# Optimization experiments

Measured on AMD Instinct MI355X. Metric: run time of the kernel, lower is better.

Reference implementation:

```python
import jax, jax.numpy as jnp
import numpy as np

B, S, D_IN, D_OUT = 4, 2048, 1024, 1024
USE_MASK = True


def setup_inputs() -> dict:
    key = jax.random.key(0)
    ks = jax.random.split(key, 6)
    return {
        "inputs_for_keys": jax.random.normal(ks[0], (B, S, D_IN), jnp.float32),
        "inputs_for_values": jax.random.normal(ks[1], (B, S, D_IN), jnp.float32),
        "inputs_for_queries": jax.random.normal(ks[2], (B, S, D_IN), jnp.float32),
        "WK": jax.random.normal(ks[3], (D_IN, D_OUT), jnp.float32) * 0.1,
        "WV": jax.random.normal(ks[4], (D_IN, D_OUT), jnp.float32) * 0.1,
        "WQ": jax.random.normal(ks[5], (D_IN, D_OUT), jnp.float32) * 0.1,
    }


def reference(inputs_for_keys, inputs_for_values, inputs_for_queries, WK, WV, WQ):
    # projections: [B,S,Din] @ [Din,Dout] -> [B,S,Dout]
    K = jnp.einsum("bsd,de->bse", inputs_for_keys, WK)
    V = jnp.einsum("bsd,de->bse", inputs_for_values, WV)
    Q = jnp.einsum("bsd,de->bse", inputs_for_queries, WQ)

    dk = jnp.asarray(K.shape[2], jnp.float32)
    # scores: [B, Sq, Sk]
    score = jnp.einsum("bqd,bkd->bqk", Q, K) / jnp.sqrt(dk)
    if USE_MASK:
        # causal: -inf strictly above diagonal (j > i), matching the
        # transposed tril(-1) * -inf construction in the original.
        q_idx = jnp.arange(S)[:, None]
        k_idx = jnp.arange(S)[None, :]
        mask = jnp.where(k_idx > q_idx, -jnp.inf, 0.0).astype(score.dtype)
        score = score + mask[None, :, :]
    soft_score = jax.nn.softmax(score, axis=-1)
    return jnp.einsum("bqk,bkd->bqd", soft_score, V)
```

## Files before the change

### kernel.cpp

```cpp
#include <hip/hip_runtime.h>
#include <hip/hip_bf16.h>

typedef unsigned short u16;
typedef _Float16 f16;
typedef __attribute__((ext_vector_type(8))) short s16x8;
typedef __attribute__((ext_vector_type(8))) _Float16 f16x8;
typedef __attribute__((ext_vector_type(4))) float f32x4;
typedef __attribute__((ext_vector_type(4))) unsigned short u16x4;

template <typename T>
__device__ __forceinline__ auto mfma_try(T a, T b, f32x4 c, int)
    -> decltype(__builtin_amdgcn_mfma_f32_16x16x32_f16(a, b, c, 0, 0, 0)) {
  return __builtin_amdgcn_mfma_f32_16x16x32_f16(a, b, c, 0, 0, 0);
}
template <typename T>
__device__ __forceinline__ f32x4 mfma_try(T a, T b, f32x4 c, long) {
  return __builtin_amdgcn_mfma_f32_16x16x32_f16(
      __builtin_bit_cast(f16x8, a), __builtin_bit_cast(f16x8, b), c, 0, 0, 0);
}
__device__ __forceinline__ f32x4 MFMA16(s16x8 a, s16x8 b, f32x4 c) {
  return mfma_try(a, b, c, 0);
}

__device__ __forceinline__ void gload16(const void* g, void* s) {
  __builtin_amdgcn_global_load_lds(
      (const __attribute__((address_space(1))) void*)g,
      (__attribute__((address_space(3))) void*)s, 16, 0, 0);
}

__device__ __forceinline__ u16 f2h(float x) {
  f16 h = (f16)x;
  u16 u;
  __builtin_memcpy(&u, &h, 2);
  return u;
}
__device__ __forceinline__ float h2f(u16 u) {
  f16 h;
  __builtin_memcpy(&h, &u, 2);
  return (float)h;
}

#define LDS_SWZ(r, cb) ((cb) ^ (((r)&7) << 4))

struct Geom {
  int srow[4], scol[4];
  int w, l, wr, wc;
};

__device__ __forceinline__ Geom make_geom() {
  Geom g;
  int tid = threadIdx.x;
  g.w = tid >> 6; g.l = tid & 63;
  g.wr = g.w >> 1; g.wc = g.w & 1;
#pragma unroll
  for (int i = 0; i < 4; ++i) {
    int off = i * 4096 + g.w * 1024 + g.l * 16;
    int r = off >> 7, cb = off & 127;
    g.srow[i] = r;
    g.scol[i] = LDS_SWZ(r, cb) >> 1;
  }
  return g;
}

__device__ __forceinline__ void stage(const u16* pan, int ld, int k0,
                                      char* lds, const Geom& g) {
#pragma unroll
  for (int i = 0; i < 4; ++i)
    gload16(pan + (long)g.srow[i] * ld + k0 + g.scol[i],
            lds + i * 4096 + g.w * 1024);
}

__device__ __forceinline__ void compute_step(const char* lA, const char* lB,
                                             const Geom& g, f32x4 acc[4][4]) {
#pragma unroll
  for (int ks = 0; ks < 2; ++ks) {
    s16x8 af[4], bg[4];
#pragma unroll
    for (int m = 0; m < 4; ++m) {
      int r = g.wr * 64 + m * 16 + (g.l & 15);
      int cb = ks * 64 + ((g.l >> 4) << 4);
      af[m] = *(const s16x8*)(lA + r * 128 + LDS_SWZ(r, cb));
    }
#pragma unroll
    for (int n = 0; n < 4; ++n) {
      int r = g.wc * 64 + n * 16 + (g.l & 15);
      int cb = ks * 64 + ((g.l >> 4) << 4);
      bg[n] = *(const s16x8*)(lB + r * 128 + LDS_SWZ(r, cb));
    }
#pragma unroll
    for (int m = 0; m < 4; ++m)
#pragma unroll
      for (int n = 0; n < 4; ++n)
        acc[m][n] = MFMA16(af[m], bg[n], acc[m][n]);
  }
}

__device__ __forceinline__ void gemm_core(const u16* Apan, int lda,
                                          const u16* Bpan, int ldb, int nsteps,
                                          char* lA, char* lB, const Geom& g,
                                          f32x4 acc[4][4]) {
  stage(Apan, lda, 0, lA, g);
  stage(Bpan, ldb, 0, lB, g);
  __syncthreads();
  for (int t = 0; t < nsteps; ++t) {
    int cur = (t & 1) << 14;
    if (t + 1 < nsteps) {
      int nxt = ((t + 1) & 1) << 14;
      stage(Apan, lda, (t + 1) * 64, lA + nxt, g);
      stage(Bpan, ldb, (t + 1) * 64, lB + nxt, g);
    }
    compute_step(lA + cur, lB + cur, g, acc);
    if (t + 1 < nsteps) __syncthreads();
  }
}

__global__ __launch_bounds__(256, 2) void proj_kernel(
    const u16* __restrict__ xk, const u16* __restrict__ xq, const u16* __restrict__ xv,
    const u16* __restrict__ wk, const u16* __restrict__ wq, const u16* __restrict__ wv,
    u16* __restrict__ K, u16* __restrict__ Q, u16* __restrict__ Vt) {
  __shared__ char lds[65536];
  const int y = blockIdx.y;
  const u16* X = y == 0 ? xk : (y == 1 ? xq : xv);
  const u16* W = y == 0 ? wk : (y == 1 ? wq : wv);
  const int bx = blockIdx.x;
  const int swz = (bx & 7) * 64 + (bx >> 3);
  const int tm = swz >> 3, tn = swz & 7;
  Geom g = make_geom();
  f32x4 acc[4][4] = {};
  gemm_core(X + (long)tm * 128 * 1024, 1024, W + (long)tn * 128 * 1024, 1024,
            16, lds, lds + 32768, g, acc);
  const int rg0 = tm * 128 + g.wr * 64, cg0 = tn * 128 + g.wc * 64;
  if (y < 2) {
    u16* C = y == 0 ? K : Q;
#pragma unroll
    for (int m = 0; m < 4; ++m)
#pragma unroll
      for (int n = 0; n < 4; ++n)
#pragma unroll
        for (int j = 0; j < 4; ++j) {
          int rg = rg0 + m * 16 + ((g.l >> 4) << 2) + j;
          int cg = cg0 + n * 16 + (g.l & 15);
          C[(long)rg * 1024 + cg] = f2h(acc[m][n][j]);
        }
  } else {
#pragma unroll
    for (int m = 0; m < 4; ++m) {
      int rg = rg0 + m * 16 + ((g.l >> 4) << 2);
      int b = rg >> 11, rl = rg & 2047;
#pragma unroll
      for (int n = 0; n < 4; ++n) {
        int cg = cg0 + n * 16 + (g.l & 15);
        u16x4 pk;
#pragma unroll
        for (int j = 0; j < 4; ++j) pk[j] = f2h(acc[m][n][j]);
        *(u16x4*)(Vt + (long)b * (1024 * 2048) + (long)cg * 2048 + rl) = pk;
      }
    }
  }
}

__global__ __launch_bounds__(256, 2) void qkt_kernel(
    const u16* __restrict__ Q, const u16* __restrict__ K, u16* __restrict__ S) {
  __shared__ char lds[65536];
  const int bx = blockIdx.x;
  const int swz = (bx & 7) * 68 + (bx >> 3);
  const int b = swz / 136;
  int t = swz - b * 136;
  int tm = 0;
  while (t > tm) { t -= tm + 1; ++tm; }
  const int tn = t;
  Geom g = make_geom();
  f32x4 acc[4][4] = {};
  const u16* Qb = Q + (long)b * 2048 * 1024;
  const u16* Kb = K + (long)b * 2048 * 1024;
  gemm_core(Qb + (long)tm * 128 * 1024, 1024, Kb + (long)tn * 128 * 1024, 1024,
            16, lds, lds + 32768, g, acc);
  u16* Sb = S + (long)b * 2048 * 2048;
  const int rg0 = tm * 128 + g.wr * 64, cg0 = tn * 128 + g.wc * 64;
#pragma unroll
  for (int m = 0; m < 4; ++m)
#pragma unroll
    for (int n = 0; n < 4; ++n)
#pragma unroll
      for (int j = 0; j < 4; ++j) {
        int rg = rg0 + m * 16 + ((g.l >> 4) << 2) + j;
        int cg = cg0 + n * 16 + (g.l & 15);
        Sb[(long)rg * 2048 + cg] = f2h(acc[m][n][j]);
      }
}

__global__ __launch_bounds__(256, 2) void pv_kernel(
    const u16* __restrict__ P, const u16* __restrict__ Vt, float* __restrict__ O) {
  __shared__ char lds[65536];
  const int bx = blockIdx.x;
  const int swz = (bx & 7) * 64 + (bx >> 3);
  const int b = swz >> 7, loc = swz & 127;
  const int tm = loc >> 3, tn = loc & 7;
  Geom g = make_geom();
  f32x4 acc[4][4] = {};
  gemm_core(P + ((long)b * 2048 + tm * 128) * 2048, 2048,
            Vt + (long)b * 1024 * 2048 + (long)tn * 128 * 2048, 2048,
            (tm + 1) * 2, lds, lds + 32768, g, acc);
  const int rg0 = tm * 128 + g.wr * 64, cg0 = tn * 128 + g.wc * 64;
#pragma unroll
  for (int m = 0; m < 4; ++m)
#pragma unroll
    for (int n = 0; n < 4; ++n)
#pragma unroll
      for (int j = 0; j < 4; ++j) {
        int rg = rg0 + m * 16 + ((g.l >> 4) << 2) + j;
        int cg = cg0 + n * 16 + (g.l & 15);
        O[((long)b * 2048 + rg) * 1024 + cg] = acc[m][n][j];
      }
}

__global__ __launch_bounds__(256) void softmax_causal(
    const u16* __restrict__ S, u16* __restrict__ P) {
  const int row = blockIdx.x;
  const int i_q = row & 2047;
  const u16* sr = S + (long)row * 2048;
  u16* pr = P + (long)row * 2048;
  const int tid = threadIdx.x;
  const int l = tid & 63, w = tid >> 6;
  const int base = tid * 8;

  s16x8 raw = *(const s16x8*)(sr + base);
  float v[8];
  float m = -INFINITY;
#pragma unroll
  for (int j = 0; j < 8; ++j) {
    float x = h2f((u16)raw[j]);
    x = (base + j <= i_q) ? x : -INFINITY;
    v[j] = x;
    m = fmaxf(m, x);
  }
  __shared__ float red[8];
  for (int o = 32; o; o >>= 1) m = fmaxf(m, __shfl_xor(m, o, 64));
  if (l == 0) red[w] = m;
  __syncthreads();
  m = fmaxf(fmaxf(red[0], red[1]), fmaxf(red[2], red[3]));

  float s = 0.f;
#pragma unroll
  for (int j = 0; j < 8; ++j) {
    v[j] = expf(v[j] - m);
    s += v[j];
  }
  for (int o = 32; o; o >>= 1) s += __shfl_xor(s, o, 64);
  if (l == 0) red[4 + w] = s;
  __syncthreads();
  s = (red[4] + red[5]) + (red[6] + red[7]);
  float inv = 1.0f / s;

  s16x8 o;
#pragma unroll
  for (int j = 0; j < 8; ++j) o[j] = (short)f2h(v[j] * inv);
  *(s16x8*)(pr + base) = o;
}

__global__ __launch_bounds__(256) void xcast_kernel(
    const float* __restrict__ x0, const float* __restrict__ x1,
    const float* __restrict__ x2, u16* __restrict__ o0, u16* __restrict__ o1,
    u16* __restrict__ o2) {
  const int y = blockIdx.y;
  const float* in = y == 0 ? x0 : (y == 1 ? x1 : x2);
  u16* out = y == 0 ? o0 : (y == 1 ? o1 : o2);
  long i = ((long)blockIdx.x * 256 + threadIdx.x) * 8;
  f32x4 a = *(const f32x4*)(in + i);
  f32x4 b = *(const f32x4*)(in + i + 4);
  s16x8 o;
#pragma unroll
  for (int j = 0; j < 4; ++j) {
    o[j] = (short)f2h(a[j]);
    o[4 + j] = (short)f2h(b[j]);
  }
  *(s16x8*)(out + i) = o;
}

__global__ __launch_bounds__(256) void wcast_kernel(
    const float* __restrict__ wk, const float* __restrict__ wv,
    const float* __restrict__ wq, u16* __restrict__ ok, u16* __restrict__ ov,
    u16* __restrict__ oq) {
  __shared__ float tile[32][33];
  const int z = blockIdx.z;
  const float* w = z == 0 ? wk : (z == 1 ? wv : wq);
  u16* o = z == 0 ? ok : (z == 1 ? ov : oq);
  const float scale = (z == 2) ? 0.03125f : 1.0f;
  const int bx = blockIdx.x, by = blockIdx.y;
  const int lx = threadIdx.x & 31, ly = threadIdx.x >> 5;
#pragma unroll
  for (int j = 0; j < 32; j += 8)
    tile[ly + j][lx] = w[(long)(by * 32 + ly + j) * 1024 + bx * 32 + lx];
  __syncthreads();
#pragma unroll
  for (int j = 0; j < 32; j += 8)
    o[(long)(bx * 32 + ly + j) * 1024 + by * 32 + lx] = f2h(tile[lx][ly + j] * scale);
}

extern "C" void kernel_launch(void* const* d_in, const int* in_sizes, int n_in,
                              void* d_out, int out_size, void* d_ws, size_t ws_size,
                              hipStream_t stream) {
  const float* Xk = (const float*)d_in[0];
  const float* Xv = (const float*)d_in[1];
  const float* Xq = (const float*)d_in[2];
  const float* WK = (const float*)d_in[3];
  const float* WV = (const float*)d_in[4];
  const float* WQ = (const float*)d_in[5];

  const int Bn = 4, S = 2048, D = 1024;
  const long NX = (long)Bn * S * D;

  const size_t r0 = (size_t)Bn * S * S * 4;
  const size_t r1 = r0 + 3ull * D * D * 2;
  const size_t r2 = r1 + 2ull * NX * 2;
  const size_t NEED = r2 + (size_t)NX * 2;
  if (ws_size < NEED) {
    hipMemsetAsync(d_out, 0, (size_t)out_size * 4, stream);
    return;
  }
  char* ws = (char*)d_ws;
  u16* xkb = (u16*)ws;
  u16* xvb = xkb + NX;
  u16* xqb = xvb + NX;
  u16* scoresH = (u16*)ws;
  u16* wkt = (u16*)(ws + r0);
  u16* wvt = wkt + D * D;
  u16* wqt = wvt + D * D;
  u16* Kb = (u16*)(ws + r1);
  u16* Qb = Kb + NX;
  u16* Pb = (u16*)(ws + r1);
  u16* Vt = (u16*)(ws + r2);

  xcast_kernel<<<dim3(4096, 3), 256, 0, stream>>>(Xk, Xv, Xq, xkb, xvb, xqb);
  wcast_kernel<<<dim3(32, 32, 3), 256, 0, stream>>>(WK, WV, WQ, wkt, wvt, wqt);
  proj_kernel<<<dim3(512, 3), 256, 0, stream>>>(xkb, xqb, xvb, wkt, wqt, wvt,
                                                Kb, Qb, Vt);
  qkt_kernel<<<dim3(544), 256, 0, stream>>>(Qb, Kb, scoresH);
  softmax_causal<<<dim3(8192), 256, 0, stream>>>(scoresH, Pb);
  pv_kernel<<<dim3(512), 256, 0, stream>>>(Pb, Vt, (float*)d_out);
}
```

Before: 163.4 us.

## Fuse input fp32->fp16 cast into projection GEMM, balance causal PV, trim softmax

The projection kernel now loads fp32 activations directly into registers, converts them to fp16 and writes them into swizzled LDS, which removes the separate xcast kernel and its round trip through global memory. The PV kernel pairs row tile p with row tile 15-p in each block, so every block does the same causal work, and it launches half as many blocks. Softmax skips loading fully masked 8-element chunks and only writes P up to the 128-column tile boundary that PV reads. The costs are more register pressure and synchronous register-staged loads in the projection, and a longer serial loop in each PV block.

```diff
diff --git a/kernel.cpp b/kernel.cpp
--- a/kernel.cpp
+++ b/kernel.cpp
@@ -43,7 +43,10 @@
 #define LDS_SWZ(r, cb) ((cb) ^ (((r)&7) << 4))
 
 struct Geom {
-  int srow[4], scol[4];
+  int srow[4];
+  int scol[4];
+  int scnat[4];
+  int wofs[4];
   int w, l, wr, wc;
 };
 
@@ -58,6 +61,8 @@
     int r = off >> 7, cb = off & 127;
     g.srow[i] = r;
     g.scol[i] = LDS_SWZ(r, cb) >> 1;
+    g.scnat[i] = cb >> 1;
+    g.wofs[i] = r * 128 + LDS_SWZ(r, cb);
   }
   return g;
 }
@@ -68,6 +73,29 @@
   for (int i = 0; i < 4; ++i)
     gload16(pan + (long)g.srow[i] * ld + k0 + g.scol[i],
             lds + i * 4096 + g.w * 1024);
+}
+
+__device__ __forceinline__ void a_issue(const float* Xpan, int k0,
+                                        const Geom& g, f32x4 (&ar)[8]) {
+#pragma unroll
+  for (int i = 0; i < 4; ++i) {
+    const float* src = Xpan + (long)g.srow[i] * 1024 + k0 + g.scnat[i];
+    ar[2 * i] = *(const f32x4*)(src);
+    ar[2 * i + 1] = *(const f32x4*)(src + 4);
+  }
+}
+__device__ __forceinline__ void a_write(char* lA, const Geom& g,
+                                        const f32x4 (&ar)[8]) {
+#pragma unroll
+  for (int i = 0; i < 4; ++i) {
+    s16x8 h;
+#pragma unroll
+    for (int j = 0; j < 4; ++j) {
+      h[j] = (short)f2h(ar[2 * i][j]);
+      h[4 + j] = (short)f2h(ar[2 * i + 1][j]);
+    }
+    *(s16x8*)(lA + g.wofs[i]) = h;
+  }
 }
 
 __device__ __forceinline__ void compute_step(const char* lA, const char* lB,
@@ -114,21 +142,46 @@
   }
 }
 
+__device__ __forceinline__ void gemm_core_xf32(const float* Xpan,
+                                               const u16* Bpan, int ldb,
+                                               int nsteps, char* lA, char* lB,
+                                               const Geom& g, f32x4 acc[4][4]) {
+  f32x4 ar[8];
+  a_issue(Xpan, 0, g, ar);
+  stage(Bpan, ldb, 0, lB, g);
+  a_write(lA, g, ar);
+  __syncthreads();
+  for (int t = 0; t < nsteps; ++t) {
+    int cur = (t & 1) << 14;
+    int nxt = ((t + 1) & 1) << 14;
+    if (t + 1 < nsteps) {
+      a_issue(Xpan, (t + 1) * 64, g, ar);
+      stage(Bpan, ldb, (t + 1) * 64, lB + nxt, g);
+    }
+    compute_step(lA + cur, lB + cur, g, acc);
+    if (t + 1 < nsteps) {
+      a_write(lA + nxt, g, ar);
+      __syncthreads();
+    }
+  }
+}
+
 __global__ __launch_bounds__(256, 2) void proj_kernel(
-    const u16* __restrict__ xk, const u16* __restrict__ xq, const u16* __restrict__ xv,
-    const u16* __restrict__ wk, const u16* __restrict__ wq, const u16* __restrict__ wv,
+    const float* __restrict__ xk, const float* __restrict__ xq,
+    const float* __restrict__ xv, const u16* __restrict__ wk,
+    const u16* __restrict__ wq, const u16* __restrict__ wv,
     u16* __restrict__ K, u16* __restrict__ Q, u16* __restrict__ Vt) {
   __shared__ char lds[65536];
   const int y = blockIdx.y;
-  const u16* X = y == 0 ? xk : (y == 1 ? xq : xv);
+  const float* X = y == 0 ? xk : (y == 1 ? xq : xv);
   const u16* W = y == 0 ? wk : (y == 1 ? wq : wv);
   const int bx = blockIdx.x;
   const int swz = (bx & 7) * 64 + (bx >> 3);
   const int tm = swz >> 3, tn = swz & 7;
   Geom g = make_geom();
   f32x4 acc[4][4] = {};
-  gemm_core(X + (long)tm * 128 * 1024, 1024, W + (long)tn * 128 * 1024, 1024,
-            16, lds, lds + 32768, g, acc);
+  gemm_core_xf32(X + (long)tm * 128 * 1024, W + (long)tn * 128 * 1024, 1024,
+                 16, lds, lds + 32768, g, acc);
   const int rg0 = tm * 128 + g.wr * 64, cg0 = tn * 128 + g.wc * 64;
   if (y < 2) {
     u16* C = y == 0 ? K : Q;
@@ -193,46 +246,56 @@
     const u16* __restrict__ P, const u16* __restrict__ Vt, float* __restrict__ O) {
   __shared__ char lds[65536];
   const int bx = blockIdx.x;
-  const int swz = (bx & 7) * 64 + (bx >> 3);
-  const int b = swz >> 7, loc = swz & 127;
-  const int tm = loc >> 3, tn = loc & 7;
+  const int swz = (bx & 7) * 32 + (bx >> 3);
+  const int b = swz >> 6, loc = swz & 63;
+  const int p = loc >> 3, tn = loc & 7;
   Geom g = make_geom();
-  f32x4 acc[4][4] = {};
-  gemm_core(P + ((long)b * 2048 + tm * 128) * 2048, 2048,
-            Vt + (long)b * 1024 * 2048 + (long)tn * 128 * 2048, 2048,
-            (tm + 1) * 2, lds, lds + 32768, g, acc);
-  const int rg0 = tm * 128 + g.wr * 64, cg0 = tn * 128 + g.wc * 64;
-#pragma unroll
-  for (int m = 0; m < 4; ++m)
-#pragma unroll
-    for (int n = 0; n < 4; ++n)
-#pragma unroll
-      for (int j = 0; j < 4; ++j) {
-        int rg = rg0 + m * 16 + ((g.l >> 4) << 2) + j;
-        int cg = cg0 + n * 16 + (g.l & 15);
-        O[((long)b * 2048 + rg) * 1024 + cg] = acc[m][n][j];
-      }
+  for (int half = 0; half < 2; ++half) {
+    const int tm = half ? (15 - p) : p;
+    f32x4 acc[4][4] = {};
+    gemm_core(P + ((long)b * 2048 + tm * 128) * 2048, 2048,
+              Vt + (long)b * 1024 * 2048 + (long)tn * 128 * 2048, 2048,
+              (tm + 1) * 2, lds, lds + 32768, g, acc);
+    const int rg0 = tm * 128 + g.wr * 64, cg0 = tn * 128 + g.wc * 64;
+#pragma unroll
+    for (int m = 0; m < 4; ++m)
+#pragma unroll
+      for (int n = 0; n < 4; ++n)
+#pragma unroll
+        for (int j = 0; j < 4; ++j) {
+          int rg = rg0 + m * 16 + ((g.l >> 4) << 2) + j;
+          int cg = cg0 + n * 16 + (g.l & 15);
+          O[((long)b * 2048 + rg) * 1024 + cg] = acc[m][n][j];
+        }
+    __syncthreads();
+  }
 }
 
 __global__ __launch_bounds__(256) void softmax_causal(
     const u16* __restrict__ S, u16* __restrict__ P) {
   const int row = blockIdx.x;
   const int i_q = row & 2047;
+  const int klim = ((i_q >> 7) + 1) << 7;
   const u16* sr = S + (long)row * 2048;
   u16* pr = P + (long)row * 2048;
   const int tid = threadIdx.x;
   const int l = tid & 63, w = tid >> 6;
   const int base = tid * 8;
 
-  s16x8 raw = *(const s16x8*)(sr + base);
   float v[8];
   float m = -INFINITY;
-#pragma unroll
-  for (int j = 0; j < 8; ++j) {
-    float x = h2f((u16)raw[j]);
-    x = (base + j <= i_q) ? x : -INFINITY;
-    v[j] = x;
-    m = fmaxf(m, x);
+  if (base <= i_q) {
+    s16x8 raw = *(const s16x8*)(sr + base);
+#pragma unroll
+    for (int j = 0; j < 8; ++j) {
+      float x = h2f((u16)raw[j]);
+      x = (base + j <= i_q) ? x : -INFINITY;
+      v[j] = x;
+      m = fmaxf(m, x);
+    }
+  } else {
+#pragma unroll
+    for (int j = 0; j < 8; ++j) v[j] = -INFINITY;
   }
   __shared__ float red[8];
   for (int o = 32; o; o >>= 1) m = fmaxf(m, __shfl_xor(m, o, 64));
@@ -252,29 +315,12 @@
   s = (red[4] + red[5]) + (red[6] + red[7]);
   float inv = 1.0f / s;
 
-  s16x8 o;
-#pragma unroll
-  for (int j = 0; j < 8; ++j) o[j] = (short)f2h(v[j] * inv);
-  *(s16x8*)(pr + base) = o;
-}
-
-__global__ __launch_bounds__(256) void xcast_kernel(
-    const float* __restrict__ x0, const float* __restrict__ x1,
-    const float* __restrict__ x2, u16* __restrict__ o0, u16* __restrict__ o1,
-    u16* __restrict__ o2) {
-  const int y = blockIdx.y;
-  const float* in = y == 0 ? x0 : (y == 1 ? x1 : x2);
-  u16* out = y == 0 ? o0 : (y == 1 ? o1 : o2);
-  long i = ((long)blockIdx.x * 256 + threadIdx.x) * 8;
-  f32x4 a = *(const f32x4*)(in + i);
-  f32x4 b = *(const f32x4*)(in + i + 4);
-  s16x8 o;
-#pragma unroll
-  for (int j = 0; j < 4; ++j) {
-    o[j] = (short)f2h(a[j]);
-    o[4 + j] = (short)f2h(b[j]);
-  }
-  *(s16x8*)(out + i) = o;
+  if (base < klim) {
+    s16x8 o;
+#pragma unroll
+    for (int j = 0; j < 8; ++j) o[j] = (short)f2h(v[j] * inv);
+    *(s16x8*)(pr + base) = o;
+  }
 }
 
 __global__ __launch_bounds__(256) void wcast_kernel(
@@ -319,9 +365,6 @@
     return;
   }
   char* ws = (char*)d_ws;
-  u16* xkb = (u16*)ws;
-  u16* xvb = xkb + NX;
-  u16* xqb = xvb + NX;
   u16* scoresH = (u16*)ws;
   u16* wkt = (u16*)(ws + r0);
   u16* wvt = wkt + D * D;
@@ -331,11 +374,10 @@
   u16* Pb = (u16*)(ws + r1);
   u16* Vt = (u16*)(ws + r2);
 
-  xcast_kernel<<<dim3(4096, 3), 256, 0, stream>>>(Xk, Xv, Xq, xkb, xvb, xqb);
   wcast_kernel<<<dim3(32, 32, 3), 256, 0, stream>>>(WK, WV, WQ, wkt, wvt, wqt);
-  proj_kernel<<<dim3(512, 3), 256, 0, stream>>>(xkb, xqb, xvb, wkt, wqt, wvt,
+  proj_kernel<<<dim3(512, 3), 256, 0, stream>>>(Xk, Xq, Xv, wkt, wqt, wvt,
                                                 Kb, Qb, Vt);
   qkt_kernel<<<dim3(544), 256, 0, stream>>>(Qb, Kb, scoresH);
   softmax_causal<<<dim3(8192), 256, 0, stream>>>(scoresH, Pb);
-  pv_kernel<<<dim3(512), 256, 0, stream>>>(Pb, Vt, (float*)d_out);
-}
+  pv_kernel<<<dim3(256), 256, 0, stream>>>(Pb, Vt, (float*)d_out);
+}
```

New measurement: 171.1 us. +4.8%, slower.
